# Performance work log

Measured on AMD Instinct MI355X. Metric: run time of the kernel, lower is better.

The kernel has to match this reference:

```python
import jax, jax.numpy as jnp
import numpy as np

N, E, F, B = 4096, 8192, 256, 16


def setup_inputs() -> dict:
    key = jax.random.key(0)
    k_x, k_idx, k_w, k_b = jax.random.split(key, 4)
    x = jax.random.normal(k_x, (B, E, F), dtype=jnp.float32)
    # Incidence matrix: each edge (column) connects 2 random distinct nodes.
    ends = jax.random.randint(k_idx, (2, E), 0, N)  # [2, E] node ids per edge
    cols = jnp.arange(E)
    inci = jnp.zeros((N, E), dtype=jnp.float32)
    inci = inci.at[ends[0], cols].set(1.0).at[ends[1], cols].set(1.0)
    w = jax.random.normal(k_w, (N, E), dtype=jnp.float32) * 0.05
    b = jax.random.normal(k_b, (N, E), dtype=jnp.float32) * 0.01
    return {"x": x, "inci": inci, "w": w, "b": b}


def reference(x, inci, w, b):
    # (w * inci + b) @ x : [N,E] x [B,E,F] -> [B,N,F]
    m = w * inci + b
    return jnp.einsum("ne,bef->bnf", m, x)
```

## Files before the change

kernel.cpp:

```cpp
#include <hip/hip_runtime.h>
#include <hip/hip_bf16.h>

#define Ndim 4096
#define Edim 8192
#define Fdim 256
#define Bdim 16
#define EB (Edim * 2)
#define NT (Edim / 64)

typedef __attribute__((ext_vector_type(8))) short bf16x8;
typedef __attribute__((ext_vector_type(4))) float f32x4;

__device__ __forceinline__ unsigned short f2bf(float f) {
  unsigned int u = __float_as_uint(f);
  u += 0x7fffu + ((u >> 16) & 1u);
  return (unsigned short)(u >> 16);
}

__device__ __forceinline__ void gload_lds16(const void* g, void* l) {
  __builtin_amdgcn_global_load_lds(
      (const __attribute__((address_space(1))) unsigned int*)g,
      (__attribute__((address_space(3))) unsigned int*)l, 16, 0, 0);
}

__device__ __forceinline__ void stage_half(const char* g, char* d) {
  gload_lds16(g, d);
  gload_lds16(g + (size_t)64 * EB, d + 8192);
}

#define RD(base, r, kk) \
  (*(const bf16x8*)((base) + (r) * 128 + ((((kk) * 64) + khi) ^ (((r) & 7) << 4))))

__global__ void convert_m(const float* __restrict__ w, const float* __restrict__ inc,
                          const float* __restrict__ bb, unsigned short* __restrict__ m) {
  size_t i = ((size_t)blockIdx.x * 256 + threadIdx.x) * 4;
  float4 wv = *(const float4*)(w + i);
  float4 iv = *(const float4*)(inc + i);
  float4 bv = *(const float4*)(bb + i);
  ushort4 o;
  o.x = f2bf(fmaf(wv.x, iv.x, bv.x));
  o.y = f2bf(fmaf(wv.y, iv.y, bv.y));
  o.z = f2bf(fmaf(wv.z, iv.z, bv.z));
  o.w = f2bf(fmaf(wv.w, iv.w, bv.w));
  *(ushort4*)(m + i) = o;
}

__global__ void transpose_x(const float* __restrict__ x, unsigned short* __restrict__ xT) {
  __shared__ unsigned short tile[64][66];
  int e0 = blockIdx.x * 64, f0 = blockIdx.y * 64, b = blockIdx.z;
  const float* xb = x + (size_t)b * Edim * Fdim;
  unsigned short* xTb = xT + (size_t)b * Fdim * Edim;
  int t = threadIdx.x;
  int fl = t & 63, rq = t >> 6;
#pragma unroll
  for (int i = 0; i < 16; i++) {
    int el = rq * 16 + i;
    float v = xb[(size_t)(e0 + el) * Fdim + f0 + fl];
    tile[el][fl] = f2bf(v);
  }
  __syncthreads();
  int ep = (t & 31) * 2;
  int fr0 = t >> 5;
#pragma unroll
  for (int j = 0; j < 8; j++) {
    int fr = fr0 + j * 8;
    unsigned int pk = (unsigned int)tile[ep][fr] | ((unsigned int)tile[ep + 1][fr] << 16);
    *(unsigned int*)&xTb[(size_t)(f0 + fr) * Edim + e0 + ep] = pk;
  }
}

template <int MODE>
__device__ __forceinline__ void ktile(
    const char* lA, const char* lB, const char* lAn, const char* lBn,
    char* d1, const char* g1, char* d2, const char* g2,
    char* d3, const char* g3, char* d4, const char* g4,
    int lane, int wr, int wc,
    bf16x8 (&aCur)[8], bf16x8 (&bLoC)[4], f32x4 acc[8][4]) {
  const int l15 = lane & 15;
  const int khi = (lane >> 4) << 4;
  bf16x8 bHi[4], aHi[8];

  if constexpr (MODE >= 1) stage_half(g1, d1);
  __builtin_amdgcn_s_barrier();
  asm volatile("s_waitcnt lgkmcnt(0)" ::: "memory");
  __builtin_amdgcn_s_setprio(1);
#pragma unroll
  for (int m = 0; m < 4; ++m)
#pragma unroll
    for (int n = 0; n < 2; ++n)
#pragma unroll
      for (int kk = 0; kk < 2; ++kk)
        acc[m][n] = __builtin_amdgcn_mfma_f32_16x16x32_bf16(aCur[m * 2 + kk], bLoC[n * 2 + kk],
                                                            acc[m][n], 0, 0, 0);
  __builtin_amdgcn_s_setprio(0);
#pragma unroll
  for (int n = 0; n < 2; ++n)
#pragma unroll
    for (int kk = 0; kk < 2; ++kk)
      bHi[n * 2 + kk] = RD(lB, wc * 64 + (n + 2) * 16 + l15, kk);
  __builtin_amdgcn_s_barrier();

  if constexpr (MODE >= 1) stage_half(g2, d2);
  __builtin_amdgcn_s_barrier();
  asm volatile("s_waitcnt lgkmcnt(0)" ::: "memory");
  __builtin_amdgcn_s_setprio(1);
#pragma unroll
  for (int m = 0; m < 4; ++m)
#pragma unroll
    for (int n = 0; n < 2; ++n)
#pragma unroll
      for (int kk = 0; kk < 2; ++kk)
        acc[m][n + 2] = __builtin_amdgcn_mfma_f32_16x16x32_bf16(aCur[m * 2 + kk], bHi[n * 2 + kk],
                                                                acc[m][n + 2], 0, 0, 0);
  __builtin_amdgcn_s_setprio(0);
#pragma unroll
  for (int m = 0; m < 4; ++m)
#pragma unroll
    for (int kk = 0; kk < 2; ++kk)
      aHi[m * 2 + kk] = RD(lA, wr * 128 + 64 + m * 16 + l15, kk);
  __builtin_amdgcn_s_barrier();

  if constexpr (MODE == 2) stage_half(g3, d3);
  __builtin_amdgcn_s_barrier();
  asm volatile("s_waitcnt lgkmcnt(0)" ::: "memory");
  __builtin_amdgcn_s_setprio(1);
#pragma unroll
  for (int m = 0; m < 4; ++m)
#pragma unroll
    for (int n = 0; n < 2; ++n)
#pragma unroll
      for (int kk = 0; kk < 2; ++kk)
        acc[m + 4][n] = __builtin_amdgcn_mfma_f32_16x16x32_bf16(aHi[m * 2 + kk], bLoC[n * 2 + kk],
                                                                acc[m + 4][n], 0, 0, 0);
  __builtin_amdgcn_s_setprio(0);
  if constexpr (MODE == 2) asm volatile("s_waitcnt vmcnt(2)" ::: "memory");
  if constexpr (MODE == 1) asm volatile("s_waitcnt vmcnt(0)" ::: "memory");
  __builtin_amdgcn_s_barrier();

  if constexpr (MODE == 2) stage_half(g4, d4);
  __builtin_amdgcn_s_barrier();
  asm volatile("s_waitcnt lgkmcnt(0)" ::: "memory");
  __builtin_amdgcn_s_setprio(1);
#pragma unroll
  for (int m = 0; m < 4; ++m)
#pragma unroll
    for (int n = 0; n < 2; ++n)
#pragma unroll
      for (int kk = 0; kk < 2; ++kk)
        acc[m + 4][n + 2] = __builtin_amdgcn_mfma_f32_16x16x32_bf16(aHi[m * 2 + kk], bHi[n * 2 + kk],
                                                                    acc[m + 4][n + 2], 0, 0, 0);
  __builtin_amdgcn_s_setprio(0);
  if constexpr (MODE >= 1) {
#pragma unroll
    for (int m = 0; m < 4; ++m)
#pragma unroll
      for (int kk = 0; kk < 2; ++kk)
        aCur[m * 2 + kk] = RD(lAn, wr * 128 + m * 16 + l15, kk);
#pragma unroll
    for (int n = 0; n < 2; ++n)
#pragma unroll
      for (int kk = 0; kk < 2; ++kk)
        bLoC[n * 2 + kk] = RD(lBn, wc * 64 + n * 16 + l15, kk);
  }
  __builtin_amdgcn_s_barrier();
}

__global__ __launch_bounds__(512, 2) void gemm8(
    const unsigned short* __restrict__ A,
    const unsigned short* __restrict__ Bt,
    float* __restrict__ C) {
  __shared__ __align__(16) char smem[131072];

  const int bid = blockIdx.x;
  const int lid = ((bid & 7) << 5) | (bid >> 3);
  const int mt = lid >> 4;
  const int bb = lid & 15;

  const int tid = threadIdx.x;
  const int lane = tid & 63;
  const int w = tid >> 6;
  const int wr = w >> 2;
  const int wc = w & 3;
  const int l15 = lane & 15;
  const int khi = (lane >> 4) << 4;

  const int r0 = tid >> 3;
  const int c0 = ((tid & 7) ^ (r0 & 7)) << 4;

  const char* Ag = (const char*)A + (size_t)(mt * 256) * EB + (size_t)r0 * EB + c0;
  const char* Bg = (const char*)Bt + (size_t)(bb * 256) * EB + (size_t)r0 * EB + c0;
  char* dst = smem + tid * 16;

  f32x4 acc[8][4];
#pragma unroll
  for (int m = 0; m < 8; ++m)
#pragma unroll
    for (int n = 0; n < 4; ++n) acc[m][n] = (f32x4){0.f, 0.f, 0.f, 0.f};

  const size_t HEB = (size_t)128 * EB;

  stage_half(Ag, dst);
  stage_half(Ag + HEB, dst + 16384);
  stage_half(Bg, dst + 32768);
  stage_half(Bg + HEB, dst + 49152);
  stage_half(Bg + 128, dst + 98304);
  stage_half(Bg + 128 + HEB, dst + 114688);
  asm volatile("s_waitcnt vmcnt(4)" ::: "memory");
  __builtin_amdgcn_s_barrier();

  bf16x8 aCur[8];
  bf16x8 bLoC[4];
#pragma unroll
  for (int m = 0; m < 4; ++m)
#pragma unroll
    for (int kk = 0; kk < 2; ++kk)
      aCur[m * 2 + kk] = RD((const char*)smem, wr * 128 + m * 16 + l15, kk);
#pragma unroll
  for (int n = 0; n < 2; ++n)
#pragma unroll
    for (int kk = 0; kk < 2; ++kk)
      bLoC[n * 2 + kk] = RD((const char*)smem + 32768, wc * 64 + n * 16 + l15, kk);

  for (int i = 0; i < NT / 2 - 1; ++i) {
    const size_t t1b = (size_t)(2 * i + 1) * 128;
    const size_t t2b = (size_t)(2 * i + 2) * 128;
    const size_t t3b = (size_t)(2 * i + 3) * 128;
    ktile<2>(smem, smem + 32768, smem + 65536, smem + 98304,
             dst + 65536, Ag + t1b,
             dst + 81920, Ag + t1b + HEB,
             dst + 32768, Bg + t2b,
             dst + 49152, Bg + t2b + HEB,
             lane, wr, wc, aCur, bLoC, acc);
    ktile<2>(smem + 65536, smem + 98304, smem, smem + 32768,
             dst, Ag + t2b,
             dst + 16384, Ag + t2b + HEB,
             dst + 98304, Bg + t3b,
             dst + 114688, Bg + t3b + HEB,
             lane, wr, wc, aCur, bLoC, acc);
  }
  {
    const size_t tlb = (size_t)(NT - 1) * 128;
    ktile<1>(smem, smem + 32768, smem + 65536, smem + 98304,
             dst + 65536, Ag + tlb,
             dst + 81920, Ag + tlb + HEB,
             nullptr, nullptr, nullptr, nullptr,
             lane, wr, wc, aCur, bLoC, acc);
    ktile<0>(smem + 65536, smem + 98304, nullptr, nullptr,
             nullptr, nullptr, nullptr, nullptr,
             nullptr, nullptr, nullptr, nullptr,
             lane, wr, wc, aCur, bLoC, acc);
  }

  float* Cb = C + (size_t)bb * (Ndim * Fdim) + (size_t)(mt * 256) * Fdim;
#pragma unroll
  for (int m = 0; m < 8; ++m) {
    int row0 = wr * 128 + m * 16 + ((lane >> 4) << 2);
#pragma unroll
    for (int n = 0; n < 4; ++n) {
      int col = wc * 64 + n * 16 + (lane & 15);
#pragma unroll
      for (int j = 0; j < 4; ++j)
        Cb[(size_t)(row0 + j) * Fdim + col] = acc[m][n][j];
    }
  }
}

__global__ void naive_kernel(const float* __restrict__ x, const float* __restrict__ inci,
                             const float* __restrict__ w, const float* __restrict__ b,
                             float* __restrict__ out) {
  int n = blockIdx.x & (Ndim - 1);
  int bb = blockIdx.x >> 12;
  int f = threadIdx.x;
  const float* xb = x + (size_t)bb * Edim * Fdim;
  const size_t nE = (size_t)n * Edim;
  float acc = 0.f;
  for (int e = 0; e < Edim; e++) {
    float m = fmaf(w[nE + e], inci[nE + e], b[nE + e]);
    acc = fmaf(m, xb[(size_t)e * Fdim + f], acc);
  }
  out[(size_t)bb * Ndim * Fdim + (size_t)n * Fdim + f] = acc;
}

extern "C" void kernel_launch(void* const* d_in, const int* in_sizes, int n_in,
                              void* d_out, int out_size, void* d_ws, size_t ws_size,
                              hipStream_t stream) {
  const float* x = (const float*)d_in[0];
  const float* inci = (const float*)d_in[1];
  const float* w = (const float*)d_in[2];
  const float* b = (const float*)d_in[3];
  float* out = (float*)d_out;

  size_t mBytes = (size_t)Ndim * Edim * 2;
  size_t xTBytes = (size_t)Bdim * Fdim * Edim * 2;
  if (ws_size >= mBytes + xTBytes) {
    unsigned short* m_bf = (unsigned short*)d_ws;
    unsigned short* xT = m_bf + (size_t)Ndim * Edim;
    convert_m<<<(Ndim * (size_t)Edim) / 4 / 256, 256, 0, stream>>>(w, inci, b, m_bf);
    transpose_x<<<dim3(Edim / 64, Fdim / 64, Bdim), 256, 0, stream>>>(x, xT);
    gemm8<<<256, 512, 0, stream>>>(m_bf, xT, out);
  } else {
    naive_kernel<<<Bdim * Ndim, 256, 0, stream>>>(x, inci, w, b, out);
  }
}
```

Before: 332.8 us.

## Switch GEMM inner loop to 32x32x16 MFMA with k-sliced LDS reads

Replaces the 16x16x32 bf16 MFMA tiling with 32x32x16 instructions, so each wave holds a 4x2 grid of 32x32 accumulators and walks the 64-wide k tile in four slices. This changes the register fragment layout, the LDS read pattern, the output store mapping and the stage ordering: all prefetches for the next tiles are now issued together in the last phase after a full vmcnt wait. The larger MFMA shape is meant to cut instruction count and LDS reads per FLOP, at the cost of less overlap between global loads and compute.

```diff
diff --git a/kernel.cpp b/kernel.cpp
--- a/kernel.cpp
+++ b/kernel.cpp
@@ -9,7 +9,7 @@
 #define NT (Edim / 64)
 
 typedef __attribute__((ext_vector_type(8))) short bf16x8;
-typedef __attribute__((ext_vector_type(4))) float f32x4;
+typedef __attribute__((ext_vector_type(16))) float f32x16;
 
 __device__ __forceinline__ unsigned short f2bf(float f) {
   unsigned int u = __float_as_uint(f);
@@ -28,8 +28,8 @@
   gload_lds16(g + (size_t)64 * EB, d + 8192);
 }
 
-#define RD(base, r, kk) \
-  (*(const bf16x8*)((base) + (r) * 128 + ((((kk) * 64) + khi) ^ (((r) & 7) << 4))))
+#define RD32(base, r, c) \
+  (*(const bf16x8*)((base) + (r) * 128 + ((((c) << 4)) ^ (((r) & 7) << 4))))
 
 __global__ void convert_m(const float* __restrict__ w, const float* __restrict__ inc,
                           const float* __restrict__ bb, unsigned short* __restrict__ m) {
@@ -75,10 +75,11 @@
     char* d1, const char* g1, char* d2, const char* g2,
     char* d3, const char* g3, char* d4, const char* g4,
     int lane, int wr, int wc,
-    bf16x8 (&aCur)[8], bf16x8 (&bLoC)[4], f32x4 acc[8][4]) {
-  const int l15 = lane & 15;
-  const int khi = (lane >> 4) << 4;
-  bf16x8 bHi[4], aHi[8];
+    bf16x8 (&aC)[4], bf16x8 (&bC)[2], f32x16 acc[4][2]) {
+  const int l31 = lane & 31;
+  const int lh = lane >> 5;
+  const int rA0 = wr * 128 + l31;
+  const int rB0 = wc * 64 + l31;
 
   if constexpr (MODE >= 1) stage_half(g1, d1);
   __builtin_amdgcn_s_barrier();
@@ -88,16 +89,12 @@
   for (int m = 0; m < 4; ++m)
 #pragma unroll
     for (int n = 0; n < 2; ++n)
-#pragma unroll
-      for (int kk = 0; kk < 2; ++kk)
-        acc[m][n] = __builtin_amdgcn_mfma_f32_16x16x32_bf16(aCur[m * 2 + kk], bLoC[n * 2 + kk],
-                                                            acc[m][n], 0, 0, 0);
-  __builtin_amdgcn_s_setprio(0);
-#pragma unroll
-  for (int n = 0; n < 2; ++n)
-#pragma unroll
-    for (int kk = 0; kk < 2; ++kk)
-      bHi[n * 2 + kk] = RD(lB, wc * 64 + (n + 2) * 16 + l15, kk);
+      acc[m][n] = __builtin_amdgcn_mfma_f32_32x32x16_bf16(aC[m], bC[n], acc[m][n], 0, 0, 0);
+  __builtin_amdgcn_s_setprio(0);
+#pragma unroll
+  for (int m = 0; m < 4; ++m) aC[m] = RD32(lA, rA0 + m * 32, 2 + lh);
+#pragma unroll
+  for (int n = 0; n < 2; ++n) bC[n] = RD32(lB, rB0 + n * 32, 2 + lh);
   __builtin_amdgcn_s_barrier();
 
   if constexpr (MODE >= 1) stage_half(g2, d2);
@@ -108,59 +105,48 @@
   for (int m = 0; m < 4; ++m)
 #pragma unroll
     for (int n = 0; n < 2; ++n)
-#pragma unroll
-      for (int kk = 0; kk < 2; ++kk)
-        acc[m][n + 2] = __builtin_amdgcn_mfma_f32_16x16x32_bf16(aCur[m * 2 + kk], bHi[n * 2 + kk],
-                                                                acc[m][n + 2], 0, 0, 0);
-  __builtin_amdgcn_s_setprio(0);
-#pragma unroll
-  for (int m = 0; m < 4; ++m)
-#pragma unroll
-    for (int kk = 0; kk < 2; ++kk)
-      aHi[m * 2 + kk] = RD(lA, wr * 128 + 64 + m * 16 + l15, kk);
-  __builtin_amdgcn_s_barrier();
-
-  if constexpr (MODE == 2) stage_half(g3, d3);
-  __builtin_amdgcn_s_barrier();
-  asm volatile("s_waitcnt lgkmcnt(0)" ::: "memory");
-  __builtin_amdgcn_s_setprio(1);
-#pragma unroll
-  for (int m = 0; m < 4; ++m)
-#pragma unroll
-    for (int n = 0; n < 2; ++n)
-#pragma unroll
-      for (int kk = 0; kk < 2; ++kk)
-        acc[m + 4][n] = __builtin_amdgcn_mfma_f32_16x16x32_bf16(aHi[m * 2 + kk], bLoC[n * 2 + kk],
-                                                                acc[m + 4][n], 0, 0, 0);
-  __builtin_amdgcn_s_setprio(0);
-  if constexpr (MODE == 2) asm volatile("s_waitcnt vmcnt(2)" ::: "memory");
-  if constexpr (MODE == 1) asm volatile("s_waitcnt vmcnt(0)" ::: "memory");
-  __builtin_amdgcn_s_barrier();
-
-  if constexpr (MODE == 2) stage_half(g4, d4);
-  __builtin_amdgcn_s_barrier();
-  asm volatile("s_waitcnt lgkmcnt(0)" ::: "memory");
-  __builtin_amdgcn_s_setprio(1);
-#pragma unroll
-  for (int m = 0; m < 4; ++m)
-#pragma unroll
-    for (int n = 0; n < 2; ++n)
-#pragma unroll
-      for (int kk = 0; kk < 2; ++kk)
-        acc[m + 4][n + 2] = __builtin_amdgcn_mfma_f32_16x16x32_bf16(aHi[m * 2 + kk], bHi[n * 2 + kk],
-                                                                    acc[m + 4][n + 2], 0, 0, 0);
+      acc[m][n] = __builtin_amdgcn_mfma_f32_32x32x16_bf16(aC[m], bC[n], acc[m][n], 0, 0, 0);
+  __builtin_amdgcn_s_setprio(0);
+#pragma unroll
+  for (int m = 0; m < 4; ++m) aC[m] = RD32(lA, rA0 + m * 32, 4 + lh);
+#pragma unroll
+  for (int n = 0; n < 2; ++n) bC[n] = RD32(lB, rB0 + n * 32, 4 + lh);
+  __builtin_amdgcn_s_barrier();
+
+  __builtin_amdgcn_s_barrier();
+  asm volatile("s_waitcnt lgkmcnt(0)" ::: "memory");
+  __builtin_amdgcn_s_setprio(1);
+#pragma unroll
+  for (int m = 0; m < 4; ++m)
+#pragma unroll
+    for (int n = 0; n < 2; ++n)
+      acc[m][n] = __builtin_amdgcn_mfma_f32_32x32x16_bf16(aC[m], bC[n], acc[m][n], 0, 0, 0);
+  __builtin_amdgcn_s_setprio(0);
+#pragma unroll
+  for (int m = 0; m < 4; ++m) aC[m] = RD32(lA, rA0 + m * 32, 6 + lh);
+#pragma unroll
+  for (int n = 0; n < 2; ++n) bC[n] = RD32(lB, rB0 + n * 32, 6 + lh);
+  if constexpr (MODE >= 1) asm volatile("s_waitcnt vmcnt(0)" ::: "memory");
+  __builtin_amdgcn_s_barrier();
+
+  __builtin_amdgcn_s_barrier();
+  asm volatile("s_waitcnt lgkmcnt(0)" ::: "memory");
+  if constexpr (MODE == 2) {
+    stage_half(g3, d3);
+    stage_half(g4, d4);
+  }
+  __builtin_amdgcn_s_setprio(1);
+#pragma unroll
+  for (int m = 0; m < 4; ++m)
+#pragma unroll
+    for (int n = 0; n < 2; ++n)
+      acc[m][n] = __builtin_amdgcn_mfma_f32_32x32x16_bf16(aC[m], bC[n], acc[m][n], 0, 0, 0);
   __builtin_amdgcn_s_setprio(0);
   if constexpr (MODE >= 1) {
 #pragma unroll
-    for (int m = 0; m < 4; ++m)
-#pragma unroll
-      for (int kk = 0; kk < 2; ++kk)
-        aCur[m * 2 + kk] = RD(lAn, wr * 128 + m * 16 + l15, kk);
-#pragma unroll
-    for (int n = 0; n < 2; ++n)
-#pragma unroll
-      for (int kk = 0; kk < 2; ++kk)
-        bLoC[n * 2 + kk] = RD(lBn, wc * 64 + n * 16 + l15, kk);
+    for (int m = 0; m < 4; ++m) aC[m] = RD32(lAn, rA0 + m * 32, 0 + lh);
+#pragma unroll
+    for (int n = 0; n < 2; ++n) bC[n] = RD32(lBn, rB0 + n * 32, 0 + lh);
   }
   __builtin_amdgcn_s_barrier();
 }
@@ -181,8 +167,8 @@
   const int w = tid >> 6;
   const int wr = w >> 2;
   const int wc = w & 3;
-  const int l15 = lane & 15;
-  const int khi = (lane >> 4) << 4;
+  const int l31 = lane & 31;
+  const int lh = lane >> 5;
 
   const int r0 = tid >> 3;
   const int c0 = ((tid & 7) ^ (r0 & 7)) << 4;
@@ -191,11 +177,13 @@
   const char* Bg = (const char*)Bt + (size_t)(bb * 256) * EB + (size_t)r0 * EB + c0;
   char* dst = smem + tid * 16;
 
-  f32x4 acc[8][4];
-#pragma unroll
-  for (int m = 0; m < 8; ++m)
-#pragma unroll
-    for (int n = 0; n < 4; ++n) acc[m][n] = (f32x4){0.f, 0.f, 0.f, 0.f};
+  f32x16 acc[4][2];
+#pragma unroll
+  for (int m = 0; m < 4; ++m)
+#pragma unroll
+    for (int n = 0; n < 2; ++n)
+#pragma unroll
+      for (int r = 0; r < 16; ++r) acc[m][n][r] = 0.f;
 
   const size_t HEB = (size_t)128 * EB;
 
@@ -208,18 +196,14 @@
   asm volatile("s_waitcnt vmcnt(4)" ::: "memory");
   __builtin_amdgcn_s_barrier();
 
-  bf16x8 aCur[8];
-  bf16x8 bLoC[4];
-#pragma unroll
-  for (int m = 0; m < 4; ++m)
-#pragma unroll
-    for (int kk = 0; kk < 2; ++kk)
-      aCur[m * 2 + kk] = RD((const char*)smem, wr * 128 + m * 16 + l15, kk);
+  bf16x8 aC[4];
+  bf16x8 bC[2];
+#pragma unroll
+  for (int m = 0; m < 4; ++m)
+    aC[m] = RD32((const char*)smem, wr * 128 + m * 32 + l31, lh);
 #pragma unroll
   for (int n = 0; n < 2; ++n)
-#pragma unroll
-    for (int kk = 0; kk < 2; ++kk)
-      bLoC[n * 2 + kk] = RD((const char*)smem + 32768, wc * 64 + n * 16 + l15, kk);
+    bC[n] = RD32((const char*)smem + 32768, wc * 64 + n * 32 + l31, lh);
 
   for (int i = 0; i < NT / 2 - 1; ++i) {
     const size_t t1b = (size_t)(2 * i + 1) * 128;
@@ -230,13 +214,13 @@
              dst + 81920, Ag + t1b + HEB,
              dst + 32768, Bg + t2b,
              dst + 49152, Bg + t2b + HEB,
-             lane, wr, wc, aCur, bLoC, acc);
+             lane, wr, wc, aC, bC, acc);
     ktile<2>(smem + 65536, smem + 98304, smem, smem + 32768,
              dst, Ag + t2b,
              dst + 16384, Ag + t2b + HEB,
              dst + 98304, Bg + t3b,
              dst + 114688, Bg + t3b + HEB,
-             lane, wr, wc, aCur, bLoC, acc);
+             lane, wr, wc, aC, bC, acc);
   }
   {
     const size_t tlb = (size_t)(NT - 1) * 128;
@@ -244,25 +228,25 @@
              dst + 65536, Ag + tlb,
              dst + 81920, Ag + tlb + HEB,
              nullptr, nullptr, nullptr, nullptr,
-             lane, wr, wc, aCur, bLoC, acc);
+             lane, wr, wc, aC, bC, acc);
     ktile<0>(smem + 65536, smem + 98304, nullptr, nullptr,
              nullptr, nullptr, nullptr, nullptr,
              nullptr, nullptr, nullptr, nullptr,
-             lane, wr, wc, aCur, bLoC, acc);
+             lane, wr, wc, aC, bC, acc);
   }
 
   float* Cb = C + (size_t)bb * (Ndim * Fdim) + (size_t)(mt * 256) * Fdim;
 #pragma unroll
-  for (int m = 0; m < 8; ++m) {
-    int row0 = wr * 128 + m * 16 + ((lane >> 4) << 2);
-#pragma unroll
-    for (int n = 0; n < 4; ++n) {
-      int col = wc * 64 + n * 16 + (lane & 15);
-#pragma unroll
-      for (int j = 0; j < 4; ++j)
-        Cb[(size_t)(row0 + j) * Fdim + col] = acc[m][n][j];
+  for (int m = 0; m < 4; ++m)
+#pragma unroll
+    for (int n = 0; n < 2; ++n) {
+      int col = wc * 64 + n * 32 + l31;
+#pragma unroll
+      for (int r = 0; r < 16; ++r) {
+        int row = wr * 128 + m * 32 + (r & 3) + ((r >> 2) << 3) + (lh << 2);
+        Cb[(size_t)row * Fdim + col] = acc[m][n][r];
+      }
     }
-  }
 }
 
 __global__ void naive_kernel(const float* __restrict__ x, const float* __restrict__ inci,
```

Result: slower. 346.0 us (+3.9%).
